# Kernel tuning notes

Hardware: AMD Instinct MI355X
Metric: run time of the kernel (lower is better)

## Reference

```python
import jax, jax.numpy as jnp
import numpy as np

NUM_HEADS = 16


def setup_inputs() -> dict:
    key = jax.random.key(0)
    ks = jax.random.split(key, 5)
    B, S, D = 4, 2048, 1024
    scale = 1.0 / np.sqrt(D)
    return {
        "x": jax.random.normal(ks[0], (B, S, D), dtype=jnp.float32),
        "q_proj": jax.random.normal(ks[1], (D, D), dtype=jnp.float32) * scale,
        "k_proj": jax.random.normal(ks[2], (D, D), dtype=jnp.float32) * scale,
        "v_proj": jax.random.normal(ks[3], (D, D), dtype=jnp.float32) * scale,
        "o_proj": jax.random.normal(ks[4], (D, D), dtype=jnp.float32) * scale,
    }


def reference(x, q_proj, k_proj, v_proj, o_proj):
    B, S, D = x.shape
    H = NUM_HEADS
    hd = D // H
    # projections: weight is [d_out, d_in]
    q = jnp.einsum('bsd,kd->bsk', x, q_proj)
    k = jnp.einsum('bsd,kd->bsk', x, k_proj)
    v = jnp.einsum('bsd,kd->bsk', x, v_proj)
    # split heads: [B, H, S, hd]
    q = q.reshape(B, S, H, hd).transpose(0, 2, 1, 3)
    k = k.reshape(B, S, H, hd).transpose(0, 2, 1, 3)
    v = v.reshape(B, S, H, hd).transpose(0, 2, 1, 3)
    scores = jnp.einsum('bhqd,bhkd->bhqk', q, k) / jnp.sqrt(jnp.asarray(hd, dtype=x.dtype))
    causal = jnp.tril(jnp.ones((S, S), dtype=bool))  # True = keep
    scores = jnp.where(causal, scores, -jnp.inf)
    attn = jax.nn.softmax(scores, axis=-1)
    out = jnp.einsum('bhqk,bhkd->bhqd', attn, v)
    out = out.transpose(0, 2, 1, 3).reshape(B, S, D)
    return jnp.einsum('bsv,mv->bsm', out, o_proj)
```

## Files before the change

### kernel.cpp

```cpp
#include <hip/hip_runtime.h>
#include <hip/hip_bf16.h>
#include <stdint.h>


typedef __bf16 bf16x8 __attribute__((ext_vector_type(8)));
typedef __bf16 bf16x4 __attribute__((ext_vector_type(4)));
typedef float  f32x4  __attribute__((ext_vector_type(4)));

static __device__ __forceinline__ f32x4 mfma16(bf16x8 a, bf16x8 b, f32x4 c) {
  return __builtin_amdgcn_mfma_f32_16x16x32_bf16(a, b, c, 0, 0, 0);
}

static __device__ __forceinline__ void load16_lds(const void* g, void* l) {
  __builtin_amdgcn_global_load_lds(
      (const __attribute__((address_space(1))) unsigned int*)g,
      (__attribute__((address_space(3))) unsigned int*)l, 16, 0, 0);
}

__global__ __launch_bounds__(256) void cvt_f32_bf16(
    const float* __restrict__ in, __bf16* __restrict__ out, int n8) {
  int i = blockIdx.x * blockDim.x + threadIdx.x;
  if (i >= n8) return;
  const float4* in4 = (const float4*)in;
  float4 a = in4[2 * i], b = in4[2 * i + 1];
  __bf16 v[8];
  v[0] = (__bf16)a.x; v[1] = (__bf16)a.y; v[2] = (__bf16)a.z; v[3] = (__bf16)a.w;
  v[4] = (__bf16)b.x; v[5] = (__bf16)b.y; v[6] = (__bf16)b.z; v[7] = (__bf16)b.w;
  *(bf16x8*)(out + 8 * i) = *(bf16x8*)v;
}

__global__ __launch_bounds__(256) void cvt_w(
    const float* __restrict__ w0, const float* __restrict__ w1,
    const float* __restrict__ w2, const float* __restrict__ w3,
    __bf16* __restrict__ wqkv, __bf16* __restrict__ wo) {
  int blk = blockIdx.x;
  int m = blk >> 9;
  const float* src = (m == 0) ? w0 : (m == 1) ? w1 : (m == 2) ? w2 : w3;
  __bf16* dst = (m < 3) ? (wqkv + (size_t)m * (1024 * 1024)) : wo;
  const float scl = (m == 0) ? 0.18033688011112042f : 1.0f;
  int i = (blk & 511) * 256 + threadIdx.x;
  const float4* in4 = (const float4*)src;
  float4 a = in4[2 * i], b = in4[2 * i + 1];
  __bf16 v[8];
  v[0] = (__bf16)(a.x * scl); v[1] = (__bf16)(a.y * scl);
  v[2] = (__bf16)(a.z * scl); v[3] = (__bf16)(a.w * scl);
  v[4] = (__bf16)(b.x * scl); v[5] = (__bf16)(b.y * scl);
  v[6] = (__bf16)(b.z * scl); v[7] = (__bf16)(b.w * scl);
  *(bf16x8*)(dst + 8 * i) = *(bf16x8*)v;
}

static __device__ __forceinline__ void stage_unit(
    const __bf16* __restrict__ X, long grow0, int K, long k0,
    __bf16* lds, int t) {
  const int lane = t & 63, w = t >> 6;
  const int rl = w * 8 + (lane >> 3);
  const int chunk = (lane & 7) ^ ((lane >> 3) & 7);
  load16_lds(X + (grow0 + rl) * (long)K + k0 + chunk * 8,
             lds + (w * 8) * 64);
}

template <typename OutT>
__global__ __launch_bounds__(512, 2) void gemm_bt8(
    const __bf16* __restrict__ A, const __bf16* __restrict__ Bw,
    OutT* __restrict__ C, int M, int N, int K, int NX) {
  __shared__ __align__(16) __bf16 As[3][256 * 64];
  __shared__ __align__(16) __bf16 Bs[3][128 * 64];
  const int t = threadIdx.x;
  const int lane = t & 63, w = t >> 6;
  const int wm = w >> 1, wn = w & 1;
  const int l15 = lane & 15, quad = lane >> 4;

  const int bid = blockIdx.x;
  const int cpx = gridDim.x >> 3;
  const int swz = (bid & 7) * cpx + (bid >> 3);
  const long m0 = (long)(swz / NX) * 256;
  const long n0 = (long)(swz % NX) * 128;

  int aoff[4][2], boff[4][2];
#pragma unroll
  for (int mf = 0; mf < 4; mf++)
#pragma unroll
    for (int ks = 0; ks < 2; ks++)
      aoff[mf][ks] = (wm * 64 + mf * 16 + l15) * 64 + (((ks * 4 + quad) ^ (l15 & 7)) << 3);
#pragma unroll
  for (int nf = 0; nf < 4; nf++)
#pragma unroll
    for (int ks = 0; ks < 2; ks++)
      boff[nf][ks] = (wn * 64 + nf * 16 + l15) * 64 + (((ks * 4 + quad) ^ (l15 & 7)) << 3);

  const int NT = K >> 6;
  __bf16 *Ac = As[0], *An = As[1], *Asg = As[2];
  __bf16 *Bc = Bs[0], *Bn = Bs[1], *Bsg = Bs[2];

#pragma unroll
  for (int u = 0; u < 4; u++) stage_unit(A, m0 + u * 64, K, 0, Ac + u * 64 * 64, t);
#pragma unroll
  for (int u = 0; u < 2; u++) stage_unit(Bw, n0 + u * 64, K, 0, Bc + u * 64 * 64, t);
#pragma unroll
  for (int u = 0; u < 4; u++) stage_unit(A, m0 + u * 64, K, 64, An + u * 64 * 64, t);
#pragma unroll
  for (int u = 0; u < 2; u++) stage_unit(Bw, n0 + u * 64, K, 64, Bn + u * 64 * 64, t);
  asm volatile("s_waitcnt vmcnt(6)" ::: "memory");
  __builtin_amdgcn_s_barrier();

  f32x4 acc[4][4] = {};
  for (int T = 0; T < NT; T++) {
    const bool pf2 = (T + 2 < NT);
    const long kn2 = (long)(T + 2) * 64;

    bf16x8 bfr[4][2];
#pragma unroll
    for (int nf = 0; nf < 4; nf++)
#pragma unroll
      for (int ks = 0; ks < 2; ks++)
        bfr[nf][ks] = *(const bf16x8*)(Bc + boff[nf][ks]);
    {
      bf16x8 a00 = *(const bf16x8*)(Ac + aoff[0][0]);
      bf16x8 a01 = *(const bf16x8*)(Ac + aoff[0][1]);
      bf16x8 a10 = *(const bf16x8*)(Ac + aoff[1][0]);
      bf16x8 a11 = *(const bf16x8*)(Ac + aoff[1][1]);
      if (pf2) {
#pragma unroll
        for (int u = 0; u < 4; u++)
          stage_unit(A, m0 + u * 64, K, kn2, Asg + u * 64 * 64, t);
      }
      __builtin_amdgcn_s_barrier();
      asm volatile("s_waitcnt lgkmcnt(0)" ::: "memory");
      __builtin_amdgcn_sched_barrier(0);
      __builtin_amdgcn_s_setprio(1);
#pragma unroll
      for (int nf = 0; nf < 4; nf++) {
        acc[0][nf] = mfma16(a00, bfr[nf][0], acc[0][nf]);
        acc[0][nf] = mfma16(a01, bfr[nf][1], acc[0][nf]);
        acc[1][nf] = mfma16(a10, bfr[nf][0], acc[1][nf]);
        acc[1][nf] = mfma16(a11, bfr[nf][1], acc[1][nf]);
      }
      __builtin_amdgcn_s_setprio(0);
      __builtin_amdgcn_s_barrier();
    }
    {
      bf16x8 a00 = *(const bf16x8*)(Ac + aoff[2][0]);
      bf16x8 a01 = *(const bf16x8*)(Ac + aoff[2][1]);
      bf16x8 a10 = *(const bf16x8*)(Ac + aoff[3][0]);
      bf16x8 a11 = *(const bf16x8*)(Ac + aoff[3][1]);
      if (pf2) {
#pragma unroll
        for (int u = 0; u < 2; u++)
          stage_unit(Bw, n0 + u * 64, K, kn2, Bsg + u * 64 * 64, t);
        asm volatile("s_waitcnt vmcnt(6)" ::: "memory");
      } else {
        asm volatile("s_waitcnt vmcnt(0)" ::: "memory");
      }
      __builtin_amdgcn_s_barrier();
      asm volatile("s_waitcnt lgkmcnt(0)" ::: "memory");
      __builtin_amdgcn_sched_barrier(0);
      __builtin_amdgcn_s_setprio(1);
#pragma unroll
      for (int nf = 0; nf < 4; nf++) {
        acc[2][nf] = mfma16(a00, bfr[nf][0], acc[2][nf]);
        acc[2][nf] = mfma16(a01, bfr[nf][1], acc[2][nf]);
        acc[3][nf] = mfma16(a10, bfr[nf][0], acc[3][nf]);
        acc[3][nf] = mfma16(a11, bfr[nf][1], acc[3][nf]);
      }
      __builtin_amdgcn_s_setprio(0);
      __builtin_amdgcn_s_barrier();
    }
    __bf16* ta = Ac; Ac = An; An = Asg; Asg = ta;
    __bf16* tb = Bc; Bc = Bn; Bn = Bsg; Bsg = tb;
  }

#pragma unroll
  for (int mf = 0; mf < 4; mf++)
#pragma unroll
    for (int nf = 0; nf < 4; nf++)
#pragma unroll
      for (int r = 0; r < 4; r++) {
        long row = m0 + wm * 64 + mf * 16 + quad * 4 + r;
        long col = n0 + wn * 64 + nf * 16 + l15;
        float v = acc[mf][nf][r];
        if constexpr (sizeof(OutT) == 2) C[row * (long)N + col] = (OutT)(__bf16)v;
        else                             C[row * (long)N + col] = v;
      }
}

__global__ __launch_bounds__(256) void vtrans(
    const __bf16* __restrict__ QKV, __bf16* __restrict__ VT) {
  constexpr int LDs = 136;
  __shared__ __align__(16) __bf16 Ts[64 * LDs];
  const int t = threadIdx.x;
  const int st0 = blockIdx.x * 128, h = blockIdx.y, b = blockIdx.z;
  const long vbase = (long)b * 2048 * 3072 + 2048 + h * 64;
#pragma unroll
  for (int i = 0; i < 4; i++) {
    int sl = i * 32 + (t >> 3), d0 = (t & 7) * 8;
    __bf16 tmp[8];
    *(uint4*)tmp = *(const uint4*)(QKV + vbase + (long)(st0 + sl) * 3072 + d0);
#pragma unroll
    for (int j = 0; j < 8; j++) Ts[(d0 + j) * LDs + sl] = tmp[j];
  }
  __syncthreads();
  const long obase = (long)(b * 16 + h) * 64 * 2048 + st0;
  const int d = t >> 2;
#pragma unroll
  for (int i = 0; i < 4; i++) {
    int sc = ((t & 3) + 4 * i) * 8;
    *(uint4*)(VT + obase + (long)d * 2048 + sc) = *(const uint4*)(Ts + d * LDs + sc);
  }
}

__global__ __launch_bounds__(256) void attn4(
    const __bf16* __restrict__ QKV, const __bf16* __restrict__ VT,
    __bf16* __restrict__ O) {
  constexpr int SD = 3072;
  constexpr int LDP = 72;
  __shared__ __align__(16) __bf16 Ks[3][64 * 64];
  __shared__ __align__(16) __bf16 Vs[3][64 * 64];
  __shared__ __align__(16) __bf16 Pw[4 * 32 * LDP];
  const int t = threadIdx.x;
  const int lane = t & 63, w = t >> 6;
  const int l15 = lane & 15, quad = lane >> 4;

  const int bid = blockIdx.x;
  const int g = (bid & 7) * 8 + (bid >> 6);
  const int jj = (bid >> 3) & 7;
  const int h = g & 15, b = g >> 4;

  const long qbase = (long)b * 2048 * SD + h * 64;
  const long kbase = qbase + 1024;
  const long vtbase = (long)(b * 16 + h) * 64 * 2048;
  __bf16* Pme = Pw + w * 32 * LDP;

  const int sr = w * 16 + (lane >> 3);
  const int scg = (lane & 7) ^ (sr & 7);
  const int ldsOff = (w * 16) * 64;
  const __bf16* gK = QKV + kbase + (long)sr * SD + scg * 8;
  const __bf16* gV = VT + vtbase + (long)sr * 2048 + scg * 8;

  int kvoff[4][2];
#pragma unroll
  for (int nt = 0; nt < 4; nt++)
#pragma unroll
    for (int kk = 0; kk < 2; kk++)
      kvoff[nt][kk] = (nt * 16 + l15) * 64 + (((kk * 4 + quad) ^ (l15 & 7)) << 3);

  bf16x8 ones;
#pragma unroll
  for (int j = 0; j < 8; j++) ones[j] = (__bf16)1.0f;

#pragma unroll
  for (int half = 0; half < 2; half++) {
    const int qt = half ? (15 - jj) : jj;
    const int q0 = qt * 128;
    const int wrow0 = q0 + w * 32;

    bf16x8 qf[2][2];
#pragma unroll
    for (int mt = 0; mt < 2; mt++)
#pragma unroll
      for (int kk = 0; kk < 2; kk++)
        qf[mt][kk] = *(const bf16x8*)(QKV + qbase +
            (long)(wrow0 + mt * 16 + l15) * SD + kk * 32 + quad * 8);

    f32x4 o_acc[2][4] = {};
    f32x4 o_l[2] = {};

    const int nkt = 2 * qt + 2;

    __syncthreads();
    load16_lds(gK, Ks[0] + ldsOff);
    load16_lds(gK + 8 * SD, Ks[0] + ldsOff + 8 * 64);
    load16_lds(gV, Vs[0] + ldsOff);
    load16_lds(gV + 8 * 2048, Vs[0] + ldsOff + 8 * 64);
    {
      const __bf16* gK1 = gK + (long)64 * SD;
      const __bf16* gV1 = gV + 64;
      load16_lds(gK1, Ks[1] + ldsOff);
      load16_lds(gK1 + 8 * SD, Ks[1] + ldsOff + 8 * 64);
      load16_lds(gV1, Vs[1] + ldsOff);
      load16_lds(gV1 + 8 * 2048, Vs[1] + ldsOff + 8 * 64);
    }

    int cur = 0;
    for (int kt = 0; kt < nkt; kt++) {
      if (kt + 1 < nkt) asm volatile("s_waitcnt vmcnt(4)" ::: "memory");
      else              asm volatile("s_waitcnt vmcnt(0)" ::: "memory");
      __builtin_amdgcn_s_barrier();
      __builtin_amdgcn_sched_barrier(0);

      if (kt + 2 < nkt) {
        int stg = cur + 2; if (stg >= 3) stg -= 3;
        const __bf16* gKn = gK + (long)(kt + 2) * 64 * SD;
        const __bf16* gVn = gV + (kt + 2) * 64;
        load16_lds(gKn, Ks[stg] + ldsOff);
        load16_lds(gKn + 8 * SD, Ks[stg] + ldsOff + 8 * 64);
        load16_lds(gVn, Vs[stg] + ldsOff);
        load16_lds(gVn + 8 * 2048, Vs[stg] + ldsOff + 8 * 64);
      }

      const int k0 = kt * 64;
      if (k0 <= wrow0 + 31) {
        const __bf16* KsB = Ks[cur];
        const __bf16* VsB = Vs[cur];
        bf16x8 kf[4][2];
#pragma unroll
        for (int nt = 0; nt < 4; nt++)
#pragma unroll
          for (int kk = 0; kk < 2; kk++)
            kf[nt][kk] = *(const bf16x8*)(KsB + kvoff[nt][kk]);
        f32x4 st[4][2];
        __builtin_amdgcn_s_setprio(1);
#pragma unroll
        for (int nt = 0; nt < 4; nt++)
#pragma unroll
          for (int mt = 0; mt < 2; mt++) {
            f32x4 z = {0.f, 0.f, 0.f, 0.f};
            z = mfma16(kf[nt][0], qf[mt][0], z);
            st[nt][mt] = mfma16(kf[nt][1], qf[mt][1], z);
          }
        __builtin_amdgcn_s_setprio(0);

        if (k0 + 63 <= wrow0) {
#pragma unroll
          for (int mt = 0; mt < 2; mt++)
#pragma unroll
            for (int nt = 0; nt < 4; nt++) {
              bf16x4 pb;
#pragma unroll
              for (int r = 0; r < 4; r++)
                pb[r] = (__bf16)__builtin_amdgcn_exp2f(st[nt][mt][r]);
              *(bf16x4*)(Pme + (mt * 16 + l15) * LDP + nt * 16 + quad * 4) = pb;
            }
        } else {
#pragma unroll
          for (int mt = 0; mt < 2; mt++) {
            const int qrow = wrow0 + mt * 16 + l15;
#pragma unroll
            for (int nt = 0; nt < 4; nt++) {
              const int keyb = k0 + nt * 16 + quad * 4;
              bf16x4 pb;
#pragma unroll
              for (int r = 0; r < 4; r++) {
                float e = __builtin_amdgcn_exp2f(st[nt][mt][r]);
                if (keyb + r > qrow) e = 0.f;
                pb[r] = (__bf16)e;
              }
              *(bf16x4*)(Pme + (mt * 16 + l15) * LDP + nt * 16 + quad * 4) = pb;
            }
          }
        }

#pragma unroll
        for (int kk = 0; kk < 2; kk++) {
          bf16x8 vf[4];
#pragma unroll
          for (int dt = 0; dt < 4; dt++)
            vf[dt] = *(const bf16x8*)(VsB + kvoff[dt][kk]);
#pragma unroll
          for (int mt = 0; mt < 2; mt++) {
            bf16x8 pf = *(const bf16x8*)(Pme + (mt * 16 + l15) * LDP + kk * 32 + quad * 8);
            __builtin_amdgcn_s_setprio(1);
#pragma unroll
            for (int dt = 0; dt < 4; dt++)
              o_acc[mt][dt] = mfma16(pf, vf[dt], o_acc[mt][dt]);
            o_l[mt] = mfma16(pf, ones, o_l[mt]);
            __builtin_amdgcn_s_setprio(0);
          }
        }
      }
      cur = (cur == 2) ? 0 : cur + 1;
    }

#pragma unroll
    for (int mt = 0; mt < 2; mt++) {
#pragma unroll
      for (int r = 0; r < 4; r++) {
        float inv = 1.f / o_l[mt][r];
        int row = wrow0 + mt * 16 + quad * 4 + r;
        long ob = ((long)b * 2048 + row) * 1024 + h * 64;
#pragma unroll
        for (int dt = 0; dt < 4; dt++)
          O[ob + dt * 16 + l15] = (__bf16)(o_acc[mt][dt][r] * inv);
      }
    }
  }
}

extern "C" void kernel_launch(void* const* d_in, const int* in_sizes, int n_in,
                              void* d_out, int out_size, void* d_ws, size_t ws_size,
                              hipStream_t stream) {
  const float* x  = (const float*)d_in[0];
  const float* wq = (const float*)d_in[1];
  const float* wk = (const float*)d_in[2];
  const float* wv = (const float*)d_in[3];
  const float* wo = (const float*)d_in[4];
  float* out = (float*)d_out;

  char* ws = (char*)d_ws;
  __bf16* xb   = (__bf16*)(ws);
  __bf16* wqkv = (__bf16*)(ws + (16l << 20));
  __bf16* wob  = (__bf16*)(ws + (22l << 20));
  __bf16* QKV  = (__bf16*)(ws + (24l << 20));
  __bf16* VT   = (__bf16*)(ws + (72l << 20));
  __bf16* Ab   = xb;

  cvt_f32_bf16<<<4096, 256, 0, stream>>>(x, xb, 8192 * 1024 / 8);
  cvt_w<<<2048, 256, 0, stream>>>(wq, wk, wv, wo, wqkv, wob);

  gemm_bt8<__bf16><<<768, 512, 0, stream>>>(xb, wqkv, QKV, 8192, 3072, 1024, 24);

  vtrans<<<dim3(16, 16, 4), 256, 0, stream>>>(QKV, VT);

  attn4<<<512, 256, 0, stream>>>(QKV, VT, Ab);

  gemm_bt8<float><<<256, 512, 0, stream>>>(Ab, wob, out, 8192, 1024, 1024, 8);
}
```

Baseline: 241.8 us.

## Add 256x256-tile ping-pong GEMM for QKV projection

Adds a new GEMM kernel that uses 256x256 output tiles with 8 waves arranged 2x4 and double-buffered LDS. Operand loads are interleaved with four MFMA phases that are fenced by barriers and raised wave priority. The fused QKV projection now launches 384 blocks through this kernel instead of 768 blocks through the 256x128 kernel. The larger tile raises data reuse per block but uses 128 KB of LDS, which with launch_bounds(512,2) may limit occupancy. The extra barriers per k-step add synchronisation cost.

```diff
diff --git a/kernel.cpp b/kernel.cpp
--- a/kernel.cpp
+++ b/kernel.cpp
@@ -60,6 +60,161 @@
 }
 
 template <typename OutT>
+__global__ __launch_bounds__(512, 2) void gemm_bt8p(
+    const __bf16* __restrict__ A, const __bf16* __restrict__ Bw,
+    OutT* __restrict__ C, int M, int N, int K, int NX) {
+  __shared__ __align__(16) __bf16 As[2][256 * 64];
+  __shared__ __align__(16) __bf16 Bs[2][256 * 64];
+  const int t = threadIdx.x;
+  const int lane = t & 63, w = t >> 6;
+  const int wm = w >> 2, wn = w & 3;
+  const int l15 = lane & 15, quad = lane >> 4;
+
+  const int bid = blockIdx.x;
+  const int cpx = gridDim.x >> 3;
+  const int swz = (bid & 7) * cpx + (bid >> 3);
+  const long m0 = (long)(swz / NX) * 256;
+  const long n0 = (long)(swz % NX) * 256;
+
+  int aoff[8][2], boff[4][2];
+#pragma unroll
+  for (int mf = 0; mf < 8; mf++)
+#pragma unroll
+    for (int ks = 0; ks < 2; ks++)
+      aoff[mf][ks] = (wm * 128 + mf * 16 + l15) * 64 + (((ks * 4 + quad) ^ (l15 & 7)) << 3);
+#pragma unroll
+  for (int nf = 0; nf < 4; nf++)
+#pragma unroll
+    for (int ks = 0; ks < 2; ks++)
+      boff[nf][ks] = (wn * 64 + nf * 16 + l15) * 64 + (((ks * 4 + quad) ^ (l15 & 7)) << 3);
+
+  const int NT = K >> 6;
+#pragma unroll
+  for (int u = 0; u < 4; u++) stage_unit(A,  m0 + u * 64, K, 0, &As[0][u * 64 * 64], t);
+#pragma unroll
+  for (int u = 0; u < 4; u++) stage_unit(Bw, n0 + u * 64, K, 0, &Bs[0][u * 64 * 64], t);
+  asm volatile("s_waitcnt vmcnt(0)" ::: "memory");
+  __builtin_amdgcn_s_barrier();
+
+  f32x4 acc[8][4] = {};
+  for (int T = 0; T < NT; T++) {
+    const int cur = T & 1;
+    __bf16* Ac = &As[cur][0];
+    __bf16* Bc = &Bs[cur][0];
+    __bf16* An = &As[cur ^ 1][0];
+    __bf16* Bn = &Bs[cur ^ 1][0];
+    const bool pf = (T + 1 < NT);
+    const long kn = (long)(T + 1) * 64;
+
+    bf16x8 bfr[4][2];
+
+    if (pf) {
+#pragma unroll
+      for (int u = 0; u < 4; u++) stage_unit(A, m0 + u * 64, K, kn, An + u * 64 * 64, t);
+    }
+#pragma unroll
+    for (int nf = 0; nf < 4; nf++)
+#pragma unroll
+      for (int ks = 0; ks < 2; ks++)
+        bfr[nf][ks] = *(const bf16x8*)(Bc + boff[nf][ks]);
+    {
+      bf16x8 a00 = *(const bf16x8*)(Ac + aoff[0][0]);
+      bf16x8 a01 = *(const bf16x8*)(Ac + aoff[0][1]);
+      bf16x8 a10 = *(const bf16x8*)(Ac + aoff[1][0]);
+      bf16x8 a11 = *(const bf16x8*)(Ac + aoff[1][1]);
+      __builtin_amdgcn_s_barrier();
+      asm volatile("s_waitcnt lgkmcnt(0)" ::: "memory");
+      __builtin_amdgcn_sched_barrier(0);
+      __builtin_amdgcn_s_setprio(1);
+#pragma unroll
+      for (int nf = 0; nf < 4; nf++) {
+        acc[0][nf] = mfma16(a00, bfr[nf][0], acc[0][nf]);
+        acc[0][nf] = mfma16(a01, bfr[nf][1], acc[0][nf]);
+        acc[1][nf] = mfma16(a10, bfr[nf][0], acc[1][nf]);
+        acc[1][nf] = mfma16(a11, bfr[nf][1], acc[1][nf]);
+      }
+      __builtin_amdgcn_s_setprio(0);
+      __builtin_amdgcn_s_barrier();
+    }
+    if (pf) {
+#pragma unroll
+      for (int u = 0; u < 4; u++) stage_unit(Bw, n0 + u * 64, K, kn, Bn + u * 64 * 64, t);
+    }
+    {
+      bf16x8 a00 = *(const bf16x8*)(Ac + aoff[2][0]);
+      bf16x8 a01 = *(const bf16x8*)(Ac + aoff[2][1]);
+      bf16x8 a10 = *(const bf16x8*)(Ac + aoff[3][0]);
+      bf16x8 a11 = *(const bf16x8*)(Ac + aoff[3][1]);
+      __builtin_amdgcn_s_barrier();
+      asm volatile("s_waitcnt lgkmcnt(0)" ::: "memory");
+      __builtin_amdgcn_sched_barrier(0);
+      __builtin_amdgcn_s_setprio(1);
+#pragma unroll
+      for (int nf = 0; nf < 4; nf++) {
+        acc[2][nf] = mfma16(a00, bfr[nf][0], acc[2][nf]);
+        acc[2][nf] = mfma16(a01, bfr[nf][1], acc[2][nf]);
+        acc[3][nf] = mfma16(a10, bfr[nf][0], acc[3][nf]);
+        acc[3][nf] = mfma16(a11, bfr[nf][1], acc[3][nf]);
+      }
+      __builtin_amdgcn_s_setprio(0);
+      __builtin_amdgcn_s_barrier();
+    }
+    {
+      bf16x8 a00 = *(const bf16x8*)(Ac + aoff[4][0]);
+      bf16x8 a01 = *(const bf16x8*)(Ac + aoff[4][1]);
+      bf16x8 a10 = *(const bf16x8*)(Ac + aoff[5][0]);
+      bf16x8 a11 = *(const bf16x8*)(Ac + aoff[5][1]);
+      __builtin_amdgcn_s_barrier();
+      asm volatile("s_waitcnt lgkmcnt(0)" ::: "memory");
+      __builtin_amdgcn_sched_barrier(0);
+      __builtin_amdgcn_s_setprio(1);
+#pragma unroll
+      for (int nf = 0; nf < 4; nf++) {
+        acc[4][nf] = mfma16(a00, bfr[nf][0], acc[4][nf]);
+        acc[4][nf] = mfma16(a01, bfr[nf][1], acc[4][nf]);
+        acc[5][nf] = mfma16(a10, bfr[nf][0], acc[5][nf]);
+        acc[5][nf] = mfma16(a11, bfr[nf][1], acc[5][nf]);
+      }
+      __builtin_amdgcn_s_setprio(0);
+      __builtin_amdgcn_s_barrier();
+    }
+    {
+      bf16x8 a00 = *(const bf16x8*)(Ac + aoff[6][0]);
+      bf16x8 a01 = *(const bf16x8*)(Ac + aoff[6][1]);
+      bf16x8 a10 = *(const bf16x8*)(Ac + aoff[7][0]);
+      bf16x8 a11 = *(const bf16x8*)(Ac + aoff[7][1]);
+      asm volatile("s_waitcnt vmcnt(0)" ::: "memory");
+      __builtin_amdgcn_s_barrier();
+      asm volatile("s_waitcnt lgkmcnt(0)" ::: "memory");
+      __builtin_amdgcn_sched_barrier(0);
+      __builtin_amdgcn_s_setprio(1);
+#pragma unroll
+      for (int nf = 0; nf < 4; nf++) {
+        acc[6][nf] = mfma16(a00, bfr[nf][0], acc[6][nf]);
+        acc[6][nf] = mfma16(a01, bfr[nf][1], acc[6][nf]);
+        acc[7][nf] = mfma16(a10, bfr[nf][0], acc[7][nf]);
+        acc[7][nf] = mfma16(a11, bfr[nf][1], acc[7][nf]);
+      }
+      __builtin_amdgcn_s_setprio(0);
+      __builtin_amdgcn_s_barrier();
+    }
+  }
+
+#pragma unroll
+  for (int mf = 0; mf < 8; mf++)
+#pragma unroll
+    for (int nf = 0; nf < 4; nf++)
+#pragma unroll
+      for (int r = 0; r < 4; r++) {
+        long row = m0 + wm * 128 + mf * 16 + quad * 4 + r;
+        long col = n0 + wn * 64 + nf * 16 + l15;
+        float v = acc[mf][nf][r];
+        if constexpr (sizeof(OutT) == 2) C[row * (long)N + col] = (OutT)(__bf16)v;
+        else                             C[row * (long)N + col] = v;
+      }
+}
+
+template <typename OutT>
 __global__ __launch_bounds__(512, 2) void gemm_bt8(
     const __bf16* __restrict__ A, const __bf16* __restrict__ Bw,
     OutT* __restrict__ C, int M, int N, int K, int NX) {
@@ -406,7 +561,7 @@
   cvt_f32_bf16<<<4096, 256, 0, stream>>>(x, xb, 8192 * 1024 / 8);
   cvt_w<<<2048, 256, 0, stream>>>(wq, wk, wv, wo, wqkv, wob);
 
-  gemm_bt8<__bf16><<<768, 512, 0, stream>>>(xb, wqkv, QKV, 8192, 3072, 1024, 24);
+  gemm_bt8p<__bf16><<<384, 512, 0, stream>>>(xb, wqkv, QKV, 8192, 3072, 1024, 12);
 
   vtrans<<<dim3(16, 16, 4), 256, 0, stream>>>(QKV, VT);
 
```

Result: slower. 257.4 us (+6.5%).

## Compute V transposed directly via swapped GEMM and merge conversion kernels

Applied to the files above, without the earlier changes.

The V projection is now computed as Wv·Xᵀ with a separate GEMM launch, which writes V already transposed ([H*hd, B*S]). The standalone transpose kernel and its extra pass over QKV are removed. The QK projection GEMM shrinks to N=2048, attention reads a 2048-wide QK buffer plus the new VT layout, and the two fp32→bf16 conversion kernels are merged into one launch. This saves a kernel launch and a read/write of V, but the swapped GEMM has a different shape (M=1024, N=8192) that may tile less efficiently.

```diff
diff --git a/kernel.cpp b/kernel.cpp
--- a/kernel.cpp
+++ b/kernel.cpp
@@ -17,36 +17,39 @@
       (__attribute__((address_space(3))) unsigned int*)l, 16, 0, 0);
 }
 
-__global__ __launch_bounds__(256) void cvt_f32_bf16(
-    const float* __restrict__ in, __bf16* __restrict__ out, int n8) {
-  int i = blockIdx.x * blockDim.x + threadIdx.x;
-  if (i >= n8) return;
-  const float4* in4 = (const float4*)in;
-  float4 a = in4[2 * i], b = in4[2 * i + 1];
-  __bf16 v[8];
-  v[0] = (__bf16)a.x; v[1] = (__bf16)a.y; v[2] = (__bf16)a.z; v[3] = (__bf16)a.w;
-  v[4] = (__bf16)b.x; v[5] = (__bf16)b.y; v[6] = (__bf16)b.z; v[7] = (__bf16)b.w;
-  *(bf16x8*)(out + 8 * i) = *(bf16x8*)v;
-}
-
-__global__ __launch_bounds__(256) void cvt_w(
+__global__ __launch_bounds__(256) void cvt_all(
+    const float* __restrict__ x,
     const float* __restrict__ w0, const float* __restrict__ w1,
     const float* __restrict__ w2, const float* __restrict__ w3,
-    __bf16* __restrict__ wqkv, __bf16* __restrict__ wo) {
-  int blk = blockIdx.x;
-  int m = blk >> 9;
-  const float* src = (m == 0) ? w0 : (m == 1) ? w1 : (m == 2) ? w2 : w3;
-  __bf16* dst = (m < 3) ? (wqkv + (size_t)m * (1024 * 1024)) : wo;
-  const float scl = (m == 0) ? 0.18033688011112042f : 1.0f;
-  int i = (blk & 511) * 256 + threadIdx.x;
-  const float4* in4 = (const float4*)src;
-  float4 a = in4[2 * i], b = in4[2 * i + 1];
-  __bf16 v[8];
-  v[0] = (__bf16)(a.x * scl); v[1] = (__bf16)(a.y * scl);
-  v[2] = (__bf16)(a.z * scl); v[3] = (__bf16)(a.w * scl);
-  v[4] = (__bf16)(b.x * scl); v[5] = (__bf16)(b.y * scl);
-  v[6] = (__bf16)(b.z * scl); v[7] = (__bf16)(b.w * scl);
-  *(bf16x8*)(dst + 8 * i) = *(bf16x8*)v;
+    __bf16* __restrict__ xb, __bf16* __restrict__ wqk,
+    __bf16* __restrict__ wvb, __bf16* __restrict__ wob) {
+  const int blk = blockIdx.x;
+  const int t = threadIdx.x;
+  if (blk < 4096) {
+    int i = blk * 256 + t;
+    const float4* in4 = (const float4*)x;
+    float4 a = in4[2 * i], b = in4[2 * i + 1];
+    __bf16 v[8];
+    v[0] = (__bf16)a.x; v[1] = (__bf16)a.y; v[2] = (__bf16)a.z; v[3] = (__bf16)a.w;
+    v[4] = (__bf16)b.x; v[5] = (__bf16)b.y; v[6] = (__bf16)b.z; v[7] = (__bf16)b.w;
+    *(bf16x8*)(xb + 8 * i) = *(bf16x8*)v;
+  } else {
+    int b2 = blk - 4096;
+    int m = b2 >> 9;
+    const float* src = (m == 0) ? w0 : (m == 1) ? w1 : (m == 2) ? w2 : w3;
+    __bf16* dst = (m == 0) ? wqk : (m == 1) ? (wqk + (size_t)(1024 * 1024))
+                : (m == 2) ? wvb : wob;
+    const float scl = (m == 0) ? 0.18033688011112042f : 1.0f;
+    int i = (b2 & 511) * 256 + t;
+    const float4* in4 = (const float4*)src;
+    float4 a = in4[2 * i], b = in4[2 * i + 1];
+    __bf16 v[8];
+    v[0] = (__bf16)(a.x * scl); v[1] = (__bf16)(a.y * scl);
+    v[2] = (__bf16)(a.z * scl); v[3] = (__bf16)(a.w * scl);
+    v[4] = (__bf16)(b.x * scl); v[5] = (__bf16)(b.y * scl);
+    v[6] = (__bf16)(b.z * scl); v[7] = (__bf16)(b.w * scl);
+    *(bf16x8*)(dst + 8 * i) = *(bf16x8*)v;
+  }
 }
 
 static __device__ __forceinline__ void stage_unit(
@@ -183,35 +186,10 @@
       }
 }
 
-__global__ __launch_bounds__(256) void vtrans(
-    const __bf16* __restrict__ QKV, __bf16* __restrict__ VT) {
-  constexpr int LDs = 136;
-  __shared__ __align__(16) __bf16 Ts[64 * LDs];
-  const int t = threadIdx.x;
-  const int st0 = blockIdx.x * 128, h = blockIdx.y, b = blockIdx.z;
-  const long vbase = (long)b * 2048 * 3072 + 2048 + h * 64;
-#pragma unroll
-  for (int i = 0; i < 4; i++) {
-    int sl = i * 32 + (t >> 3), d0 = (t & 7) * 8;
-    __bf16 tmp[8];
-    *(uint4*)tmp = *(const uint4*)(QKV + vbase + (long)(st0 + sl) * 3072 + d0);
-#pragma unroll
-    for (int j = 0; j < 8; j++) Ts[(d0 + j) * LDs + sl] = tmp[j];
-  }
-  __syncthreads();
-  const long obase = (long)(b * 16 + h) * 64 * 2048 + st0;
-  const int d = t >> 2;
-#pragma unroll
-  for (int i = 0; i < 4; i++) {
-    int sc = ((t & 3) + 4 * i) * 8;
-    *(uint4*)(VT + obase + (long)d * 2048 + sc) = *(const uint4*)(Ts + d * LDs + sc);
-  }
-}
-
 __global__ __launch_bounds__(256) void attn4(
-    const __bf16* __restrict__ QKV, const __bf16* __restrict__ VT,
+    const __bf16* __restrict__ QK, const __bf16* __restrict__ VT,
     __bf16* __restrict__ O) {
-  constexpr int SD = 3072;
+  constexpr int SD = 2048;
   constexpr int LDP = 72;
   __shared__ __align__(16) __bf16 Ks[3][64 * 64];
   __shared__ __align__(16) __bf16 Vs[3][64 * 64];
@@ -227,14 +205,13 @@
 
   const long qbase = (long)b * 2048 * SD + h * 64;
   const long kbase = qbase + 1024;
-  const long vtbase = (long)(b * 16 + h) * 64 * 2048;
   __bf16* Pme = Pw + w * 32 * LDP;
 
   const int sr = w * 16 + (lane >> 3);
   const int scg = (lane & 7) ^ (sr & 7);
   const int ldsOff = (w * 16) * 64;
-  const __bf16* gK = QKV + kbase + (long)sr * SD + scg * 8;
-  const __bf16* gV = VT + vtbase + (long)sr * 2048 + scg * 8;
+  const __bf16* gK = QK + kbase + (long)sr * SD + scg * 8;
+  const __bf16* gV = VT + (long)(h * 64 + sr) * 8192 + b * 2048 + scg * 8;
 
   int kvoff[4][2];
 #pragma unroll
@@ -258,7 +235,7 @@
     for (int mt = 0; mt < 2; mt++)
 #pragma unroll
       for (int kk = 0; kk < 2; kk++)
-        qf[mt][kk] = *(const bf16x8*)(QKV + qbase +
+        qf[mt][kk] = *(const bf16x8*)(QK + qbase +
             (long)(wrow0 + mt * 16 + l15) * SD + kk * 32 + quad * 8);
 
     f32x4 o_acc[2][4] = {};
@@ -270,14 +247,14 @@
     load16_lds(gK, Ks[0] + ldsOff);
     load16_lds(gK + 8 * SD, Ks[0] + ldsOff + 8 * 64);
     load16_lds(gV, Vs[0] + ldsOff);
-    load16_lds(gV + 8 * 2048, Vs[0] + ldsOff + 8 * 64);
+    load16_lds(gV + 8 * 8192, Vs[0] + ldsOff + 8 * 64);
     {
       const __bf16* gK1 = gK + (long)64 * SD;
       const __bf16* gV1 = gV + 64;
       load16_lds(gK1, Ks[1] + ldsOff);
       load16_lds(gK1 + 8 * SD, Ks[1] + ldsOff + 8 * 64);
       load16_lds(gV1, Vs[1] + ldsOff);
-      load16_lds(gV1 + 8 * 2048, Vs[1] + ldsOff + 8 * 64);
+      load16_lds(gV1 + 8 * 8192, Vs[1] + ldsOff + 8 * 64);
     }
 
     int cur = 0;
@@ -294,7 +271,7 @@
         load16_lds(gKn, Ks[stg] + ldsOff);
         load16_lds(gKn + 8 * SD, Ks[stg] + ldsOff + 8 * 64);
         load16_lds(gVn, Vs[stg] + ldsOff);
-        load16_lds(gVn + 8 * 2048, Vs[stg] + ldsOff + 8 * 64);
+        load16_lds(gVn + 8 * 8192, Vs[stg] + ldsOff + 8 * 64);
       }
 
       const int k0 = kt * 64;
@@ -397,20 +374,20 @@
 
   char* ws = (char*)d_ws;
   __bf16* xb   = (__bf16*)(ws);
-  __bf16* wqkv = (__bf16*)(ws + (16l << 20));
+  __bf16* wqk  = (__bf16*)(ws + (16l << 20));
+  __bf16* wvb  = (__bf16*)(ws + (20l << 20));
   __bf16* wob  = (__bf16*)(ws + (22l << 20));
-  __bf16* QKV  = (__bf16*)(ws + (24l << 20));
-  __bf16* VT   = (__bf16*)(ws + (72l << 20));
+  __bf16* QK   = (__bf16*)(ws + (24l << 20));
+  __bf16* VTg  = (__bf16*)(ws + (56l << 20));
   __bf16* Ab   = xb;
 
-  cvt_f32_bf16<<<4096, 256, 0, stream>>>(x, xb, 8192 * 1024 / 8);
-  cvt_w<<<2048, 256, 0, stream>>>(wq, wk, wv, wo, wqkv, wob);
-
-  gemm_bt8<__bf16><<<768, 512, 0, stream>>>(xb, wqkv, QKV, 8192, 3072, 1024, 24);
-
-  vtrans<<<dim3(16, 16, 4), 256, 0, stream>>>(QKV, VT);
-
-  attn4<<<512, 256, 0, stream>>>(QKV, VT, Ab);
+  cvt_all<<<6144, 256, 0, stream>>>(x, wq, wk, wv, wo, xb, wqk, wvb, wob);
+
+  gemm_bt8<__bf16><<<512, 512, 0, stream>>>(xb, wqk, QK, 8192, 2048, 1024, 16);
+
+  gemm_bt8<__bf16><<<256, 512, 0, stream>>>(wvb, xb, VTg, 1024, 8192, 1024, 64);
+
+  attn4<<<512, 256, 0, stream>>>(QK, VTg, Ab);
 
   gemm_bt8<float><<<256, 512, 0, stream>>>(Ab, wob, out, 8192, 1024, 1024, 8);
 }
```

Measured after the change: 229.5 us. 5.1% less time.
